# Optimization experiments

Measured on AMD Instinct MI355X. Metric: run time of the kernel, lower is better.

The kernel has to match this reference:

```python
import jax, jax.numpy as jnp
import numpy as np

B, T, D, R = 4, 2048, 512, 1024
N_INNER, N_B = 9, 2          # inner pool bins, boundary pool bins (roipool_size='2_9')
RATIO = 1.0 / 5.0            # boundary extension ratio passed to BRoI1DPool
NB = N_B + N_INNER + N_B     # 13 total bins: [start bins | inner bins | end bins]


def _bin_centers(a, b, n):
    # a, b: (B, R) -> (B, R, n) centers of n equal bins covering [a, b]
    i = (jnp.arange(n, dtype=a.dtype) + 0.5) / n
    return a[..., None] + i * (b - a)[..., None]


def broi1d_pool(feats, rois):
    # Boundary ROI 1D pooling: feats (B, T, D), rois (B, R, 2) -> (B, R, D, NB).
    # Each bin samples its center position via linear interpolation along T.
    s, e = rois[..., 0], rois[..., 1]
    ext = RATIO * (e - s)
    pos = jnp.concatenate([
        _bin_centers(s - ext, s + ext, N_B),
        _bin_centers(s, e, N_INNER),
        _bin_centers(e - ext, e + ext, N_B)], axis=-1)          # (B, R, NB)
    pos = jnp.clip(pos, 0.0, T - 1)
    lo = jnp.floor(pos).astype(jnp.int32)
    hi = jnp.minimum(lo + 1, T - 1)
    w = (pos - lo.astype(pos.dtype))[..., None]

    def gather(idx):
        g = jnp.take_along_axis(feats, idx.reshape(idx.shape[0], -1)[..., None], axis=1)
        return g.reshape(idx.shape + (feats.shape[-1],))          # (B, R, NB, D)

    vals = (1.0 - w) * gather(lo) + w * gather(hi)
    return vals.transpose(0, 1, 3, 2)                              # (B, R, D, NB)


def setup_inputs():
    key = jax.random.key(0)
    ks = jax.random.split(key, 10)
    features = jax.random.normal(ks[0], (B, T, D), jnp.float32)

    def make_rois(k):
        k1, k2 = jax.random.split(k)
        s = jax.random.uniform(k1, (B, R), jnp.float32, 0.0, T - 300.0)
        L = 16.0 + jax.random.uniform(k2, (B, R), jnp.float32) * 256.0
        return jnp.stack([s, s + L], axis=-1)

    rois = make_rois(ks[1])
    start_rois = make_rois(ks[2])
    end_rois = make_rois(ks[3])
    rois_mask = jnp.ones((B, R), jnp.float32)
    rois_pos_emb = jax.random.normal(ks[4], (B, R, D), jnp.float32)

    d_left = (N_B + N_INNER // 2 + 1) * D
    W_left = jax.random.normal(ks[5], (D, d_left), jnp.float32) / np.sqrt(d_left).astype(np.float32)
    b_left = jnp.zeros((D,), jnp.float32)
    W_inner = jax.random.normal(ks[6], (D, N_INNER * D), jnp.float32) / np.sqrt(N_INNER * D).astype(np.float32)
    b_inner = jnp.zeros((D,), jnp.float32)
    W_roi = jax.random.normal(ks[7], (D, 2 * D), jnp.float32) / np.sqrt(2 * D).astype(np.float32)
    b_roi = jnp.zeros((D,), jnp.float32)
    return {"features": features, "start_rois": start_rois, "end_rois": end_rois,
            "rois": rois, "rois_mask": rois_mask, "rois_pos_emb": rois_pos_emb,
            "W_left": W_left, "b_left": b_left, "W_inner": W_inner, "b_inner": b_inner,
            "W_roi": W_roi, "b_roi": b_roi}


def reference(features, start_rois, end_rois, rois, rois_mask, rois_pos_emb,
              W_left, b_left, W_inner, b_inner, W_roi, b_roi):
    pooled = broi1d_pool(features, rois)          # (B, R, D, NB)
    mb, r = pooled.shape[:2]

    def fc(x, W, b):
        # Linear + Dropout(eval=identity) + SELU
        return jax.nn.selu(x @ W.T + b)

    left = fc(pooled[:, :, :, 0:N_INNER // 2 + N_B + 1].reshape(mb, r, -1), W_left, b_left)
    inner = fc(pooled[:, :, :, N_B:N_INNER + N_B].reshape(mb, r, -1), W_inner, b_inner)
    # NOTE: the original code reuses left_fc for the right branch (right_fc is dead).
    right = fc(pooled[:, :, :, N_INNER // 2 + N_B:N_INNER + 2 * N_B].reshape(mb, r, -1), W_left, b_left)
    return fc(jnp.concatenate([right - left, inner], axis=2), W_roi, b_roi)  # (B, R, D)
```

## Files before the change

kernel.cpp:

```cpp
#include <hip/hip_runtime.h>
#include <hip/hip_bf16.h>
#include <cstdint>
#include <cmath>

#define BB 4
#define TT 2048
#define DD 512
#define RR 1024
#define MM (BB*RR)
#define NBINS 13
#define LDXP (NBINS*DD)

typedef __bf16 bf16;
typedef bf16 bf16x8 __attribute__((ext_vector_type(8)));
typedef bf16 bf16x2 __attribute__((ext_vector_type(2)));
typedef float f32x4 __attribute__((ext_vector_type(4)));

__device__ __forceinline__ float selu_f(float x) {
    const float sc = 1.0507009873554805f;
    const float aa = 1.6732632423543772f;
    return x > 0.0f ? sc * x : sc * aa * (expf(x) - 1.0f);
}

__device__ __forceinline__ void gload_lds16(const bf16* g, bf16* l) {
    __builtin_amdgcn_global_load_lds(
        (const __attribute__((address_space(1))) void*)g,
        (__attribute__((address_space(3))) void*)l, 16, 0, 0);
}

template<int N>
__device__ __forceinline__ void wait_vm() {
    if constexpr (N == 0)      asm volatile("s_waitcnt vmcnt(0)" ::: "memory");
    else if constexpr (N == 6) asm volatile("s_waitcnt vmcnt(6)" ::: "memory");
    else if constexpr (N == 8) asm volatile("s_waitcnt vmcnt(8)" ::: "memory");
}

template<int ROWS>
__device__ __forceinline__ void stage_tile64(const bf16* __restrict__ src, int lda,
                                             bf16* tile, int tid) {
#pragma unroll
    for (int it = 0; it < ROWS / 32; ++it) {
        int idx = it * 256 + tid;
        int row = idx >> 3;
        int col = ((idx & 7) ^ (row & 7)) * 8;
        bf16* wavebase = tile + (idx & ~63) * 8;
        gload_lds16(src + (size_t)row * lda + col, wavebase);
    }
}

__device__ __forceinline__ bf16x8 frd64(const bf16* tile, int row, int s) {
    int p = s ^ (row & 7);
    return *(const bf16x8*)(tile + row * 64 + p * 8);
}

template<int NB_, int KT>
__device__ __forceinline__ void w_row_body(const float* __restrict__ Wsrc,
                                           bf16* __restrict__ Wdst,
                                           float* ld, int n, int tid) {
    const float* src = Wsrc + (size_t)n * KT;
    for (int i = tid; i < KT; i += 256) ld[i] = src[i];
    __syncthreads();
    bf16* dst = Wdst + (size_t)n * KT;
    for (int i = tid; i < KT; i += 256) {
        int bin = i >> 9, d = i & 511;
        dst[i] = (bf16)ld[d * NB_ + bin];
    }
}

__device__ __forceinline__ void pool_body(const float* __restrict__ feats,
                                          const float* __restrict__ rois,
                                          bf16* __restrict__ Xp, int m, int tid) {
    int b = m >> 10;
    float s = rois[2 * m];
    float e = rois[2 * m + 1];
    float ext = 0.2f * (e - s);
    int d0 = tid * 2;
    bf16* orow = Xp + (size_t)m * LDXP + d0;
    const float* fb = feats + (size_t)b * TT * DD + d0;
#pragma unroll
    for (int j = 0; j < NBINS; ++j) {
        float pos;
        if (j < 2)       pos = (s - ext) + ((float)j + 0.5f) * ext;
        else if (j < 11) pos = s + (((float)(j - 2) + 0.5f) * (1.0f / 9.0f)) * (e - s);
        else             pos = (e - ext) + ((float)(j - 11) + 0.5f) * ext;
        pos = fminf(fmaxf(pos, 0.0f), (float)(TT - 1));
        float fl = floorf(pos);
        int lo = (int)fl;
        int hi = lo + 1; if (hi > TT - 1) hi = TT - 1;
        float w = pos - fl;
        float2 vlo = *(const float2*)(fb + (size_t)lo * DD);
        float2 vhi = *(const float2*)(fb + (size_t)hi * DD);
        bf16x2 o;
        o.x = (bf16)((1.0f - w) * vlo.x + w * vhi.x);
        o.y = (bf16)((1.0f - w) * vlo.y + w * vhi.y);
        *(bf16x2*)(orow + j * DD) = o;
    }
}

__global__ __launch_bounds__(256) void prep_all(
    const float* __restrict__ feats, const float* __restrict__ rois,
    const float* __restrict__ W_left, const float* __restrict__ W_inner,
    const float* __restrict__ W_roi,
    bf16* __restrict__ Xp, bf16* __restrict__ Wl, bf16* __restrict__ Wi,
    bf16* __restrict__ Wr)
{
    __shared__ float ld[4608];
    int bid = blockIdx.x, tid = threadIdx.x;
    if (bid < 4096) {
        pool_body(feats, rois, Xp, bid, tid);
    } else if (bid < 4608) {
        w_row_body<7, 3584>(W_left, Wl, ld, bid - 4096, tid);
    } else if (bid < 5120) {
        w_row_body<9, 4608>(W_inner, Wi, ld, bid - 4608, tid);
    } else {
        int i0 = (bid - 5120) * 1024 + tid * 4;
        float4 v = *(const float4*)(W_roi + i0);
        bf16* d = Wr + i0;
        d[0] = (bf16)v.x; d[1] = (bf16)v.y; d[2] = (bf16)v.z; d[3] = (bf16)v.w;
    }
}


template<int K, bool OUT_BF16>
__device__ __forceinline__ void gemm_single_body(
    const bf16* __restrict__ A, int lda,
    const bf16* __restrict__ Bw, const float* __restrict__ bias,
    void* __restrict__ Out, int ldo, int ocol0,
    bf16* sm, int m0, int n0)
{
    int tid = threadIdx.x, lane = tid & 63, w = tid >> 6;
    int wr = w >> 1, wc = w & 1;
    const bf16* Ab = A + (size_t)m0 * lda;
    const bf16* Bb = Bw + (size_t)n0 * K;
    int frow = lane & 15, sl = lane >> 4;
    f32x4 acc[2][4] = {};
    bf16 *A0 = sm,         *B0 = sm + 4096;
    bf16 *A1 = sm + 12288, *B1 = sm + 12288 + 4096;

    auto stage = [&](bf16* as, bf16* bs, int t) {
        stage_tile64<64>(Ab + t * 64, lda, as, tid);
        stage_tile64<128>(Bb + t * 64, K, bs, tid);
    };
    auto step_body = [&](bf16* as, bf16* bs, int t, bool dostage) {
        __builtin_amdgcn_s_barrier();
        bf16x8 af[2][2], bfr[2][4];
#pragma unroll
        for (int ks = 0; ks < 2; ++ks) {
#pragma unroll
            for (int mf = 0; mf < 2; ++mf) af[ks][mf] = frd64(as, wr * 32 + mf * 16 + frow, ks * 4 + sl);
#pragma unroll
            for (int nf = 0; nf < 4; ++nf) bfr[ks][nf] = frd64(bs, wc * 64 + nf * 16 + frow, ks * 4 + sl);
        }
        asm volatile("s_waitcnt lgkmcnt(0)" ::: "memory");
        __builtin_amdgcn_sched_barrier(0);
        __builtin_amdgcn_s_barrier();
        if (dostage) stage(as, bs, t + 2);
        __builtin_amdgcn_s_setprio(1);
#pragma unroll
        for (int ks = 0; ks < 2; ++ks)
#pragma unroll
            for (int mf = 0; mf < 2; ++mf)
#pragma unroll
                for (int nf = 0; nf < 4; ++nf)
                    acc[mf][nf] = __builtin_amdgcn_mfma_f32_16x16x32_bf16(af[ks][mf], bfr[ks][nf], acc[mf][nf], 0, 0, 0);
        __builtin_amdgcn_s_setprio(0);
    };

    constexpr int NT = K / 64;
    stage(A0, B0, 0);
    stage(A1, B1, 1);
    for (int t = 0; t + 2 < NT; t += 2) {
        wait_vm<6>(); step_body(A0, B0, t, true);
        wait_vm<6>(); step_body(A1, B1, t + 1, true);
    }
    wait_vm<6>(); step_body(A0, B0, NT - 2, false);
    wait_vm<0>(); step_body(A1, B1, NT - 1, false);

    int crow = (lane >> 4) * 4;
    int ccol = lane & 15;
#pragma unroll
    for (int mf = 0; mf < 2; ++mf) {
#pragma unroll
        for (int nf = 0; nf < 4; ++nf) {
            int col = n0 + wc * 64 + nf * 16 + ccol;
            float bv = bias[col];
#pragma unroll
            for (int r2 = 0; r2 < 4; ++r2) {
                int row = m0 + wr * 32 + mf * 16 + crow + r2;
                float v = selu_f(acc[mf][nf][r2] + bv);
                if constexpr (OUT_BF16)
                    ((bf16*)Out)[(size_t)row * ldo + ocol0 + col] = (bf16)v;
                else
                    ((float*)Out)[(size_t)row * ldo + ocol0 + col] = v;
            }
        }
    }
}

template<int K>
__device__ __forceinline__ void gemm_dual_body(
    const bf16* __restrict__ Xp, const bf16* __restrict__ Wl,
    const float* __restrict__ bias, bf16* __restrict__ Y,
    bf16* sm, int m0, int n0)
{
    int tid = threadIdx.x, lane = tid & 63, w = tid >> 6;
    int wr = w >> 1, wc = w & 1;
    const bf16* AL = Xp + (size_t)m0 * LDXP;
    const bf16* AR = AL + 3072;
    const bf16* Bb = Wl + (size_t)n0 * K;
    int frow = lane & 15, sl = lane >> 4;
    f32x4 accL[2][4] = {}, accR[2][4] = {};
    bf16 *L0 = sm,         *R0 = sm + 4096,         *B0 = sm + 8192;
    bf16 *L1 = sm + 16384, *R1 = sm + 16384 + 4096, *B1 = sm + 16384 + 8192;

    auto stage = [&](bf16* ls, bf16* rs, bf16* bs, int t) {
        stage_tile64<64>(AL + t * 64, LDXP, ls, tid);
        stage_tile64<64>(AR + t * 64, LDXP, rs, tid);
        stage_tile64<128>(Bb + t * 64, K, bs, tid);
    };
    auto step_body = [&](bf16* ls, bf16* rs, bf16* bs, int t, bool dostage) {
        __builtin_amdgcn_s_barrier();
        bf16x8 afL[2][2], afR[2][2], bfr[2][4];
#pragma unroll
        for (int ks = 0; ks < 2; ++ks) {
#pragma unroll
            for (int mf = 0; mf < 2; ++mf) {
                afL[ks][mf] = frd64(ls, wr * 32 + mf * 16 + frow, ks * 4 + sl);
                afR[ks][mf] = frd64(rs, wr * 32 + mf * 16 + frow, ks * 4 + sl);
            }
#pragma unroll
            for (int nf = 0; nf < 4; ++nf) bfr[ks][nf] = frd64(bs, wc * 64 + nf * 16 + frow, ks * 4 + sl);
        }
        asm volatile("s_waitcnt lgkmcnt(0)" ::: "memory");
        __builtin_amdgcn_sched_barrier(0);
        __builtin_amdgcn_s_barrier();
        if (dostage) stage(ls, rs, bs, t + 2);
        __builtin_amdgcn_s_setprio(1);
#pragma unroll
        for (int ks = 0; ks < 2; ++ks)
#pragma unroll
            for (int mf = 0; mf < 2; ++mf)
#pragma unroll
                for (int nf = 0; nf < 4; ++nf) {
                    accL[mf][nf] = __builtin_amdgcn_mfma_f32_16x16x32_bf16(afL[ks][mf], bfr[ks][nf], accL[mf][nf], 0, 0, 0);
                    accR[mf][nf] = __builtin_amdgcn_mfma_f32_16x16x32_bf16(afR[ks][mf], bfr[ks][nf], accR[mf][nf], 0, 0, 0);
                }
        __builtin_amdgcn_s_setprio(0);
    };

    constexpr int NT = K / 64;
    stage(L0, R0, B0, 0);
    stage(L1, R1, B1, 1);
    for (int t = 0; t + 2 < NT; t += 2) {
        wait_vm<8>(); step_body(L0, R0, B0, t, true);
        wait_vm<8>(); step_body(L1, R1, B1, t + 1, true);
    }
    wait_vm<8>(); step_body(L0, R0, B0, NT - 2, false);
    wait_vm<0>(); step_body(L1, R1, B1, NT - 1, false);

    int crow = (lane >> 4) * 4;
    int ccol = lane & 15;
#pragma unroll
    for (int mf = 0; mf < 2; ++mf) {
#pragma unroll
        for (int nf = 0; nf < 4; ++nf) {
            int col = n0 + wc * 64 + nf * 16 + ccol;
            float bv = bias[col];
#pragma unroll
            for (int r2 = 0; r2 < 4; ++r2) {
                int row = m0 + wr * 32 + mf * 16 + crow + r2;
                float vL = selu_f(accL[mf][nf][r2] + bv);
                float vR = selu_f(accR[mf][nf][r2] + bv);
                Y[(size_t)row * 1024 + col] = (bf16)(vR - vL);
            }
        }
    }
}

__global__ __launch_bounds__(256) void wide_gemm(
    const bf16* __restrict__ Xp, const bf16* __restrict__ Wl,
    const float* __restrict__ bl, const bf16* __restrict__ Wi,
    const float* __restrict__ bi, bf16* __restrict__ Y)
{
    __shared__ bf16 sm[32768];
    int bid = blockIdx.x;
    if (bid < 256) {
        gemm_dual_body<3584>(Xp, Wl, bl, Y, sm, (bid & 63) * 64, (bid >> 6) * 128);
    } else {
        int b2 = bid - 256;
        gemm_single_body<4608, true>(Xp + 1024, LDXP, Wi, bi, (void*)Y, 1024, 512,
                                     sm, (b2 & 63) * 64, (b2 >> 6) * 128);
    }
}

__global__ __launch_bounds__(256) void final_gemm(
    const bf16* __restrict__ Y, const bf16* __restrict__ Wr,
    const float* __restrict__ br, float* __restrict__ out)
{
    __shared__ bf16 sm[24576];
    int bid = blockIdx.x;
    gemm_single_body<1024, false>(Y, 1024, Wr, br, (void*)out, 512, 0,
                                  sm, (bid & 63) * 64, (bid >> 6) * 128);
}

extern "C" void kernel_launch(void* const* d_in, const int* in_sizes, int n_in,
                              void* d_out, int out_size, void* d_ws, size_t ws_size,
                              hipStream_t stream) {
    const float* feats   = (const float*)d_in[0];
    const float* rois    = (const float*)d_in[3];
    const float* W_left  = (const float*)d_in[6];
    const float* b_left  = (const float*)d_in[7];
    const float* W_inner = (const float*)d_in[8];
    const float* b_inner = (const float*)d_in[9];
    const float* W_roi   = (const float*)d_in[10];
    const float* b_roi   = (const float*)d_in[11];
    float* out = (float*)d_out;

    bf16* wsb = (bf16*)d_ws;
    constexpr size_t XP_ELEMS = (size_t)MM * LDXP;
    constexpr size_t WL_ELEMS = (size_t)512 * 3584;
    constexpr size_t WI_ELEMS = (size_t)512 * 4608;
    constexpr size_t WR_ELEMS = (size_t)512 * 1024;
    bf16* Xp = wsb;
    bf16* Wl = Xp + XP_ELEMS;
    bf16* Wi = Wl + WL_ELEMS;
    bf16* Wr = Wi + WI_ELEMS;
    bf16* Y  = Wr + WR_ELEMS;

    prep_all<<<5632, 256, 0, stream>>>(feats, rois, W_left, W_inner, W_roi,
                                       Xp, Wl, Wi, Wr);
    wide_gemm<<<512, 256, 0, stream>>>(Xp, Wl, b_left, Wi, b_inner, Y);
    final_gemm<<<256, 256, 0, stream>>>(Y, Wr, b_roi, out);
}
```

Measured before the change: 104.0 us.

## Load GEMM weight fragments directly into registers instead of staging through LDS

The weight (B) operand of both the wide and final GEMMs is now loaded from global memory straight into register fragments, double-buffered one k-step ahead, instead of being staged into LDS and read back. Only the activation tiles still go through LDS, which shrinks shared memory per block, and the launch bounds now request two blocks per CU. The vmcnt waits are updated for the changed number of outstanding loads. In exchange each wave fetches its own B fragments with no reuse across the wave rows (wr), so global/L2 traffic for B doubles and register pressure rises.

```diff
diff --git a/kernel.cpp b/kernel.cpp
--- a/kernel.cpp
+++ b/kernel.cpp
@@ -30,9 +30,10 @@
 
 template<int N>
 __device__ __forceinline__ void wait_vm() {
-    if constexpr (N == 0)      asm volatile("s_waitcnt vmcnt(0)" ::: "memory");
-    else if constexpr (N == 6) asm volatile("s_waitcnt vmcnt(6)" ::: "memory");
-    else if constexpr (N == 8) asm volatile("s_waitcnt vmcnt(8)" ::: "memory");
+    if constexpr (N == 0)       asm volatile("s_waitcnt vmcnt(0)" ::: "memory");
+    else if constexpr (N == 8)  asm volatile("s_waitcnt vmcnt(8)" ::: "memory");
+    else if constexpr (N == 10) asm volatile("s_waitcnt vmcnt(10)" ::: "memory");
+    else if constexpr (N == 12) asm volatile("s_waitcnt vmcnt(12)" ::: "memory");
 }
 
 template<int ROWS>
@@ -131,30 +132,41 @@
     int tid = threadIdx.x, lane = tid & 63, w = tid >> 6;
     int wr = w >> 1, wc = w & 1;
     const bf16* Ab = A + (size_t)m0 * lda;
-    const bf16* Bb = Bw + (size_t)n0 * K;
     int frow = lane & 15, sl = lane >> 4;
     f32x4 acc[2][4] = {};
-    bf16 *A0 = sm,         *B0 = sm + 4096;
-    bf16 *A1 = sm + 12288, *B1 = sm + 12288 + 4096;
-
-    auto stage = [&](bf16* as, bf16* bs, int t) {
-        stage_tile64<64>(Ab + t * 64, lda, as, tid);
-        stage_tile64<128>(Bb + t * 64, K, bs, tid);
-    };
-    auto step_body = [&](bf16* as, bf16* bs, int t, bool dostage) {
+    bf16 *A0 = sm, *A1 = sm + 4096;
+
+    const bf16* Brow[4];
+#pragma unroll
+    for (int nf = 0; nf < 4; ++nf)
+        Brow[nf] = Bw + (size_t)(n0 + wc * 64 + nf * 16 + frow) * K + sl * 8;
+
+    auto stageA = [&](bf16* ap, int t) {
+        stage_tile64<64>(Ab + t * 64, lda, ap, tid);
+    };
+    auto loadB = [&](bf16x8 (&dst)[2][4], int t) {
+#pragma unroll
+        for (int ks = 0; ks < 2; ++ks)
+#pragma unroll
+            for (int nf = 0; nf < 4; ++nf)
+                dst[ks][nf] = *(const bf16x8*)(Brow[nf] + t * 64 + ks * 32);
+    };
+    bf16x8 b0[2][4], b1[2][4];
+
+    auto step = [&](bf16* ap, bf16x8 (&bc)[2][4], bf16x8 (&bn)[2][4],
+                    int t, bool doB, bool doStage) {
         __builtin_amdgcn_s_barrier();
-        bf16x8 af[2][2], bfr[2][4];
-#pragma unroll
-        for (int ks = 0; ks < 2; ++ks) {
-#pragma unroll
-            for (int mf = 0; mf < 2; ++mf) af[ks][mf] = frd64(as, wr * 32 + mf * 16 + frow, ks * 4 + sl);
-#pragma unroll
-            for (int nf = 0; nf < 4; ++nf) bfr[ks][nf] = frd64(bs, wc * 64 + nf * 16 + frow, ks * 4 + sl);
-        }
+        bf16x8 af[2][2];
+#pragma unroll
+        for (int ks = 0; ks < 2; ++ks)
+#pragma unroll
+            for (int mf = 0; mf < 2; ++mf)
+                af[ks][mf] = frd64(ap, wr * 32 + mf * 16 + frow, ks * 4 + sl);
         asm volatile("s_waitcnt lgkmcnt(0)" ::: "memory");
         __builtin_amdgcn_sched_barrier(0);
         __builtin_amdgcn_s_barrier();
-        if (dostage) stage(as, bs, t + 2);
+        if (doB) loadB(bn, t + 1);
+        if (doStage) stageA(ap, t + 2);
         __builtin_amdgcn_s_setprio(1);
 #pragma unroll
         for (int ks = 0; ks < 2; ++ks)
@@ -162,19 +174,20 @@
             for (int mf = 0; mf < 2; ++mf)
 #pragma unroll
                 for (int nf = 0; nf < 4; ++nf)
-                    acc[mf][nf] = __builtin_amdgcn_mfma_f32_16x16x32_bf16(af[ks][mf], bfr[ks][nf], acc[mf][nf], 0, 0, 0);
+                    acc[mf][nf] = __builtin_amdgcn_mfma_f32_16x16x32_bf16(af[ks][mf], bc[ks][nf], acc[mf][nf], 0, 0, 0);
         __builtin_amdgcn_s_setprio(0);
     };
 
     constexpr int NT = K / 64;
-    stage(A0, B0, 0);
-    stage(A1, B1, 1);
+    stageA(A0, 0);
+    stageA(A1, 1);
+    loadB(b0, 0);
     for (int t = 0; t + 2 < NT; t += 2) {
-        wait_vm<6>(); step_body(A0, B0, t, true);
-        wait_vm<6>(); step_body(A1, B1, t + 1, true);
-    }
-    wait_vm<6>(); step_body(A0, B0, NT - 2, false);
-    wait_vm<0>(); step_body(A1, B1, NT - 1, false);
+        wait_vm<10>(); step(A0, b0, b1, t,     true, true);
+        wait_vm<10>(); step(A1, b1, b0, t + 1, true, true);
+    }
+    wait_vm<10>(); step(A0, b0, b1, NT - 2, true, false);
+    wait_vm<8>();  step(A1, b1, b0, NT - 1, false, false);
 
     int crow = (lane >> 4) * 4;
     int ccol = lane & 15;
@@ -207,34 +220,44 @@
     int wr = w >> 1, wc = w & 1;
     const bf16* AL = Xp + (size_t)m0 * LDXP;
     const bf16* AR = AL + 3072;
-    const bf16* Bb = Wl + (size_t)n0 * K;
     int frow = lane & 15, sl = lane >> 4;
     f32x4 accL[2][4] = {}, accR[2][4] = {};
-    bf16 *L0 = sm,         *R0 = sm + 4096,         *B0 = sm + 8192;
-    bf16 *L1 = sm + 16384, *R1 = sm + 16384 + 4096, *B1 = sm + 16384 + 8192;
-
-    auto stage = [&](bf16* ls, bf16* rs, bf16* bs, int t) {
-        stage_tile64<64>(AL + t * 64, LDXP, ls, tid);
-        stage_tile64<64>(AR + t * 64, LDXP, rs, tid);
-        stage_tile64<128>(Bb + t * 64, K, bs, tid);
-    };
-    auto step_body = [&](bf16* ls, bf16* rs, bf16* bs, int t, bool dostage) {
+    bf16 *L0 = sm, *R0 = sm + 4096, *L1 = sm + 8192, *R1 = sm + 12288;
+
+    const bf16* Brow[4];
+#pragma unroll
+    for (int nf = 0; nf < 4; ++nf)
+        Brow[nf] = Wl + (size_t)(n0 + wc * 64 + nf * 16 + frow) * K + sl * 8;
+
+    auto stageA = [&](bf16* lp, bf16* rp, int t) {
+        stage_tile64<64>(AL + t * 64, LDXP, lp, tid);
+        stage_tile64<64>(AR + t * 64, LDXP, rp, tid);
+    };
+    auto loadB = [&](bf16x8 (&dst)[2][4], int t) {
+#pragma unroll
+        for (int ks = 0; ks < 2; ++ks)
+#pragma unroll
+            for (int nf = 0; nf < 4; ++nf)
+                dst[ks][nf] = *(const bf16x8*)(Brow[nf] + t * 64 + ks * 32);
+    };
+    bf16x8 b0[2][4], b1[2][4];
+
+    auto step = [&](bf16* lp, bf16* rp, bf16x8 (&bc)[2][4], bf16x8 (&bn)[2][4],
+                    int t, bool doB, bool doStage) {
         __builtin_amdgcn_s_barrier();
-        bf16x8 afL[2][2], afR[2][2], bfr[2][4];
-#pragma unroll
-        for (int ks = 0; ks < 2; ++ks) {
+        bf16x8 afL[2][2], afR[2][2];
+#pragma unroll
+        for (int ks = 0; ks < 2; ++ks)
 #pragma unroll
             for (int mf = 0; mf < 2; ++mf) {
-                afL[ks][mf] = frd64(ls, wr * 32 + mf * 16 + frow, ks * 4 + sl);
-                afR[ks][mf] = frd64(rs, wr * 32 + mf * 16 + frow, ks * 4 + sl);
+                afL[ks][mf] = frd64(lp, wr * 32 + mf * 16 + frow, ks * 4 + sl);
+                afR[ks][mf] = frd64(rp, wr * 32 + mf * 16 + frow, ks * 4 + sl);
             }
-#pragma unroll
-            for (int nf = 0; nf < 4; ++nf) bfr[ks][nf] = frd64(bs, wc * 64 + nf * 16 + frow, ks * 4 + sl);
-        }
         asm volatile("s_waitcnt lgkmcnt(0)" ::: "memory");
         __builtin_amdgcn_sched_barrier(0);
         __builtin_amdgcn_s_barrier();
-        if (dostage) stage(ls, rs, bs, t + 2);
+        if (doB) loadB(bn, t + 1);
+        if (doStage) stageA(lp, rp, t + 2);
         __builtin_amdgcn_s_setprio(1);
 #pragma unroll
         for (int ks = 0; ks < 2; ++ks)
@@ -242,21 +265,22 @@
             for (int mf = 0; mf < 2; ++mf)
 #pragma unroll
                 for (int nf = 0; nf < 4; ++nf) {
-                    accL[mf][nf] = __builtin_amdgcn_mfma_f32_16x16x32_bf16(afL[ks][mf], bfr[ks][nf], accL[mf][nf], 0, 0, 0);
-                    accR[mf][nf] = __builtin_amdgcn_mfma_f32_16x16x32_bf16(afR[ks][mf], bfr[ks][nf], accR[mf][nf], 0, 0, 0);
+                    accL[mf][nf] = __builtin_amdgcn_mfma_f32_16x16x32_bf16(afL[ks][mf], bc[ks][nf], accL[mf][nf], 0, 0, 0);
+                    accR[mf][nf] = __builtin_amdgcn_mfma_f32_16x16x32_bf16(afR[ks][mf], bc[ks][nf], accR[mf][nf], 0, 0, 0);
                 }
         __builtin_amdgcn_s_setprio(0);
     };
 
     constexpr int NT = K / 64;
-    stage(L0, R0, B0, 0);
-    stage(L1, R1, B1, 1);
+    stageA(L0, R0, 0);
+    stageA(L1, R1, 1);
+    loadB(b0, 0);
     for (int t = 0; t + 2 < NT; t += 2) {
-        wait_vm<8>(); step_body(L0, R0, B0, t, true);
-        wait_vm<8>(); step_body(L1, R1, B1, t + 1, true);
-    }
-    wait_vm<8>(); step_body(L0, R0, B0, NT - 2, false);
-    wait_vm<0>(); step_body(L1, R1, B1, NT - 1, false);
+        wait_vm<12>(); step(L0, R0, b0, b1, t,     true, true);
+        wait_vm<12>(); step(L1, R1, b1, b0, t + 1, true, true);
+    }
+    wait_vm<12>(); step(L0, R0, b0, b1, NT - 2, true, false);
+    wait_vm<8>();  step(L1, R1, b1, b0, NT - 1, false, false);
 
     int crow = (lane >> 4) * 4;
     int ccol = lane & 15;
@@ -277,12 +301,12 @@
     }
 }
 
-__global__ __launch_bounds__(256) void wide_gemm(
+__global__ __launch_bounds__(256, 2) void wide_gemm(
     const bf16* __restrict__ Xp, const bf16* __restrict__ Wl,
     const float* __restrict__ bl, const bf16* __restrict__ Wi,
     const float* __restrict__ bi, bf16* __restrict__ Y)
 {
-    __shared__ bf16 sm[32768];
+    __shared__ bf16 sm[16384];
     int bid = blockIdx.x;
     if (bid < 256) {
         gemm_dual_body<3584>(Xp, Wl, bl, Y, sm, (bid & 63) * 64, (bid >> 6) * 128);
@@ -293,11 +317,11 @@
     }
 }
 
-__global__ __launch_bounds__(256) void final_gemm(
+__global__ __launch_bounds__(256, 2) void final_gemm(
     const bf16* __restrict__ Y, const bf16* __restrict__ Wr,
     const float* __restrict__ br, float* __restrict__ out)
 {
-    __shared__ bf16 sm[24576];
+    __shared__ bf16 sm[8192];
     int bid = blockIdx.x;
     gemm_single_body<1024, false>(Y, 1024, Wr, br, (void*)out, 512, 0,
                                   sm, (bid & 63) * 64, (bid >> 6) * 128);
```

Result: slower. 199.5 us (+91.9%).
